# Performance work log

Hardware: AMD Instinct MI355X
Metric: run time of the kernel (lower is better)

The kernel has to match this reference:

```python
import jax, jax.numpy as jnp
import numpy as np

B, S, D, H = 2, 2048, 1024, 16
HD = D // H


def setup_inputs() -> dict:
    key = jax.random.key(0)
    ks = jax.random.split(key, 9)
    std = 0.02
    return {
        "x": jax.random.normal(ks[0], (B, S, D), dtype=jnp.float32),
        "wq": jax.random.normal(ks[1], (D, D), dtype=jnp.float32) * std,
        "bq": jnp.zeros((D,), dtype=jnp.float32),
        "wk": jax.random.normal(ks[2], (D, D), dtype=jnp.float32) * std,
        "bk": jnp.zeros((D,), dtype=jnp.float32),
        "wv": jax.random.normal(ks[3], (D, D), dtype=jnp.float32) * std,
        "bv": jnp.zeros((D,), dtype=jnp.float32),
        "wo": jax.random.normal(ks[4], (D, D), dtype=jnp.float32) * std,
        "bo": jnp.zeros((D,), dtype=jnp.float32),
    }


def reference(x, wq, bq, wk, bk, wv, bv, wo, bo):
    bsz, seq_len, d_model = x.shape
    # projections: torch Linear computes x @ W.T + b with W of shape (out, in)
    q = (x @ wq.T + bq).reshape(bsz, seq_len, H, HD).transpose(0, 2, 1, 3)  # bhsd
    k = (x @ wk.T + bk).reshape(bsz, seq_len, H, HD).transpose(0, 2, 1, 3)
    v = (x @ wv.T + bv).reshape(bsz, seq_len, H, HD).transpose(0, 2, 1, 3)
    scale = HD ** -0.5
    scores = jnp.einsum("bhqd,bhkd->bhqk", q, k) * scale  # [B,H,S,S]
    causal = jnp.tril(jnp.ones((seq_len, seq_len), dtype=bool))
    scores = jnp.where(causal[None, None], scores, -jnp.inf)
    attn = jax.nn.softmax(scores, axis=-1)
    ctx = jnp.einsum("bhqk,bhkd->bhqd", attn, v)
    ctx = ctx.transpose(0, 2, 1, 3).reshape(bsz, seq_len, d_model)
    return ctx @ wo.T + bo
```

## Files before the change

### kernel.cpp

```cpp
#include <hip/hip_runtime.h>
#include <hip/hip_bf16.h>

#define B_  2
#define S_  2048
#define D_  1024
#define H_  16
#define HD_ 64
#define M_  (B_ * S_)

typedef __bf16 bf16;
typedef __bf16 bf16x8 __attribute__((ext_vector_type(8)));
typedef float  f32x4  __attribute__((ext_vector_type(4)));

__device__ __forceinline__ bf16x8 ld8g(const bf16* p) { return *(const bf16x8*)p; }

#define GLL(g, l) __builtin_amdgcn_global_load_lds( \
    (const __attribute__((address_space(1))) void*)(g), \
    (__attribute__((address_space(3))) void*)(l), 16, 0, 0)

__global__ __launch_bounds__(256) void convert_kernel(
    const float* __restrict__ x,  const float* __restrict__ wq,
    const float* __restrict__ wk, const float* __restrict__ wv,
    const float* __restrict__ wo,
    bf16* __restrict__ xb,  bf16* __restrict__ wqb, bf16* __restrict__ wkb,
    bf16* __restrict__ wvb, bf16* __restrict__ wob)
{
    const int seg = blockIdx.y;
    const float* src;
    bf16* dst;
    if (seg < 4)      { src = x  + (long)seg * 1048576; dst = xb  + (long)seg * 1048576; }
    else if (seg == 4){ src = wq; dst = wqb; }
    else if (seg == 5){ src = wk; dst = wkb; }
    else if (seg == 6){ src = wv; dst = wvb; }
    else              { src = wo; dst = wob; }
    const long i = ((long)blockIdx.x * 256 + threadIdx.x) * 8;
    float4 a = *(const float4*)(src + i);
    float4 b = *(const float4*)(src + i + 4);
    bf16x8 r;
    r[0] = (bf16)a.x; r[1] = (bf16)a.y; r[2] = (bf16)a.z; r[3] = (bf16)a.w;
    r[4] = (bf16)b.x; r[5] = (bf16)b.y; r[6] = (bf16)b.z; r[7] = (bf16)b.w;
    *(bf16x8*)(dst + i) = r;
}

template <typename TOUT>
__device__ __forceinline__ void gemm_core(
    const bf16* __restrict__ A, const bf16* __restrict__ Bt,
    const float* __restrict__ bias, TOUT* __restrict__ Cout)
{
    __shared__ bf16 As[128 * 32];
    __shared__ bf16 Bs[128 * 32];

    const int tid  = threadIdx.x;
    const int wave = tid >> 6;
    const int lane = tid & 63;
    const int quad = lane >> 4;
    const int l15  = lane & 15;
    const int wr   = (wave >> 1) * 64;
    const int wc   = (wave & 1) * 64;
    const int m0   = blockIdx.y * 128;
    const int n0   = blockIdx.x * 128;

    const int sr = wave * 16 + (lane >> 2);
    const int sc = (lane & 3) * 8;
    const bf16* Ag = A  + (long)(m0 + sr) * D_ + sc;
    const bf16* Bg = Bt + (long)(n0 + sr) * D_ + sc;
    bf16* lA = As + wave * 512;
    bf16* lB = Bs + wave * 512;

    f32x4 acc[4][4] = {};

    for (int k0 = 0; k0 < D_; k0 += 32) {
        __syncthreads();
        GLL(Ag + k0,             lA);
        GLL(Ag + 64 * D_ + k0,   lA + 64 * 32);
        GLL(Bg + k0,             lB);
        GLL(Bg + 64 * D_ + k0,   lB + 64 * 32);
        __syncthreads();

        bf16x8 af[4], bfr[4];
        for (int mi = 0; mi < 4; mi++)
            af[mi] = *(const bf16x8*)&As[(wr + mi * 16 + l15) * 32 + quad * 8];
        for (int ni = 0; ni < 4; ni++)
            bfr[ni] = *(const bf16x8*)&Bs[(wc + ni * 16 + l15) * 32 + quad * 8];

        for (int mi = 0; mi < 4; mi++)
            for (int ni = 0; ni < 4; ni++)
                acc[mi][ni] = __builtin_amdgcn_mfma_f32_16x16x32_bf16(
                    af[mi], bfr[ni], acc[mi][ni], 0, 0, 0);
    }

    for (int ni = 0; ni < 4; ni++) {
        const int col = n0 + wc + ni * 16 + l15;
        const float bv = bias[col];
        for (int mi = 0; mi < 4; mi++) {
            const int rowb = m0 + wr + mi * 16 + quad * 4;
            for (int r = 0; r < 4; r++)
                Cout[(long)(rowb + r) * D_ + col] = (TOUT)(acc[mi][ni][r] + bv);
        }
    }
}

__global__ __launch_bounds__(256) void gemm_qkv(
    const bf16* __restrict__ xb,
    const bf16* __restrict__ wqb, const bf16* __restrict__ wkb, const bf16* __restrict__ wvb,
    const float* __restrict__ bq, const float* __restrict__ bk, const float* __restrict__ bv,
    bf16* __restrict__ qb, bf16* __restrict__ kb, bf16* __restrict__ vb)
{
    const bf16*  W  = (blockIdx.z == 0) ? wqb : (blockIdx.z == 1) ? wkb : wvb;
    const float* bi = (blockIdx.z == 0) ? bq  : (blockIdx.z == 1) ? bk  : bv;
    bf16*        o  = (blockIdx.z == 0) ? qb  : (blockIdx.z == 1) ? kb  : vb;
    gemm_core<bf16>(xb, W, bi, o);
}

__global__ __launch_bounds__(256) void gemm_out(
    const bf16* __restrict__ cb, const bf16* __restrict__ wob,
    const float* __restrict__ bo, float* __restrict__ out)
{
    gemm_core<float>(cb, wob, bo, out);
}

__global__ __launch_bounds__(256) void transpose_v(
    const bf16* __restrict__ vb, bf16* __restrict__ vt)
{
    __shared__ bf16 T[64 * 72];
    const int tid = threadIdx.x;
    const int bh  = blockIdx.y;
    const int st  = blockIdx.x;
    const int b   = bh >> 4, h = bh & 15;

    const bf16* src = vb + ((long)b * S_ + st * 64) * D_ + h * 64;
    const int r = tid >> 3;
    const int c = (tid & 7) * 8;
    bf16x8 u0 = ld8g(src + (long)r * D_ + c);
    bf16x8 u1 = ld8g(src + (long)(r + 32) * D_ + c);
    *(bf16x8*)&T[r * 72 + c]        = u0;
    *(bf16x8*)&T[(r + 32) * 72 + c] = u1;
    __syncthreads();

    for (int pass = 0; pass < 2; pass++) {
        const int hd = (tid >> 3) + pass * 32;
        const int s0 = (tid & 7) * 8;
        bf16x8 o;
        for (int e = 0; e < 8; e++) o[e] = T[(s0 + e) * 72 + hd];
        *(bf16x8*)&vt[((long)bh * 64 + hd) * S_ + st * 64 + s0] = o;
    }
}

__global__ __launch_bounds__(512) void attn_kernel(
    const bf16* __restrict__ Q, const bf16* __restrict__ K,
    const bf16* __restrict__ vt, bf16* __restrict__ ctx)
{
    constexpr int LDK = 72;
    __shared__ bf16 Ks[64 * LDK];
    __shared__ bf16 Vt[64 * LDK];
    __shared__ bf16 Pq[8][16 * LDK];

    const int tid  = threadIdx.x;
    const int wave = tid >> 6;
    const int lane = tid & 63;
    const int quad = lane >> 4;
    const int l15  = lane & 15;
    const int bh   = blockIdx.y;
    const int b    = bh >> 4, h = bh & 15;
    const long base  = ((long)b * S_) * D_ + h * HD_;
    const bf16* Vth  = vt + (long)bh * 64 * S_;

    const int krow = tid >> 3;
    const int kcol = (tid & 7) * 8;

    for (int phase = 0; phase < 2; phase++) {
        const int qt = phase ? (15 - blockIdx.x) : blockIdx.x;
        const int qw    = qt * 128 + wave * 16;
        const int qrow  = qw + l15;
        const bf16* Qr = Q + base + (long)qrow * D_;
        bf16x8 qf0 = ld8g(&Qr[quad * 8]);
        bf16x8 qf1 = ld8g(&Qr[quad * 8 + 32]);

        float l_i = 0.f;
        f32x4 o_acc[4] = {};

        bf16x8 k0 = ld8g(K + base + (long)krow * D_ + kcol);
        bf16x8 w0 = ld8g(Vth + (long)krow * S_ + kcol);

        const int njt = 2 * qt + 2;
        for (int j = 0; j < njt; j++) {
            const int kbase = j * 64;
            __syncthreads();
            *(bf16x8*)&Ks[krow * LDK + kcol] = k0;
            *(bf16x8*)&Vt[krow * LDK + kcol] = w0;
            __syncthreads();

            if (j + 1 < njt) {
                k0 = ld8g(K + base + (long)(kbase + 64 + krow) * D_ + kcol);
                w0 = ld8g(Vth + (long)krow * S_ + kbase + 64 + kcol);
            }

            if (kbase <= qw + 15) {
                f32x4 sc[4];
                for (int kt = 0; kt < 4; kt++) {
                    const bf16* Kr = &Ks[(kt * 16 + l15) * LDK + quad * 8];
                    bf16x8 a0 = *(const bf16x8*)Kr;
                    bf16x8 a1 = *(const bf16x8*)(Kr + 32);
                    f32x4 z = {};
                    z = __builtin_amdgcn_mfma_f32_16x16x32_bf16(a0, qf0, z, 0, 0, 0);
                    z = __builtin_amdgcn_mfma_f32_16x16x32_bf16(a1, qf1, z, 0, 0, 0);
                    sc[kt] = z;
                }
                float sum = 0.f;
                if (kbase + 63 > qw) {
                    for (int kt = 0; kt < 4; kt++)
                        for (int r = 0; r < 4; r++) {
                            const int k_g = kbase + kt * 16 + quad * 4 + r;
                            const float p = (k_g <= qrow)
                                ? __expf(sc[kt][r] * 0.125f) : 0.f;
                            sc[kt][r] = p;
                            sum += p;
                        }
                } else {
                    for (int kt = 0; kt < 4; kt++)
                        for (int r = 0; r < 4; r++) {
                            const float p = __expf(sc[kt][r] * 0.125f);
                            sc[kt][r] = p;
                            sum += p;
                        }
                }
                sum += __shfl_xor(sum, 16, 64);
                sum += __shfl_xor(sum, 32, 64);
                l_i += sum;

                bf16* Pw = &Pq[wave][0];
                for (int kt = 0; kt < 4; kt++) {
                    union { uint2 u; bf16 hh[4]; } pk;
                    pk.hh[0] = (bf16)sc[kt][0];
                    pk.hh[1] = (bf16)sc[kt][1];
                    pk.hh[2] = (bf16)sc[kt][2];
                    pk.hh[3] = (bf16)sc[kt][3];
                    *(uint2*)&Pw[l15 * LDK + kt * 16 + quad * 4] = pk.u;
                }
                __asm__ volatile("s_waitcnt lgkmcnt(0)" ::: "memory");
                bf16x8 pf0 = *(const bf16x8*)&Pw[l15 * LDK + quad * 8];
                bf16x8 pf1 = *(const bf16x8*)&Pw[l15 * LDK + quad * 8 + 32];

                for (int ni = 0; ni < 4; ni++) {
                    const bf16* Vr = &Vt[(ni * 16 + l15) * LDK + quad * 8];
                    bf16x8 av0 = *(const bf16x8*)Vr;
                    bf16x8 av1 = *(const bf16x8*)(Vr + 32);
                    o_acc[ni] = __builtin_amdgcn_mfma_f32_16x16x32_bf16(av0, pf0, o_acc[ni], 0, 0, 0);
                    o_acc[ni] = __builtin_amdgcn_mfma_f32_16x16x32_bf16(av1, pf1, o_acc[ni], 0, 0, 0);
                }
            }
        }

        const float invl = 1.f / l_i;
        bf16* Pw = &Pq[wave][0];
        for (int ni = 0; ni < 4; ni++)
            for (int r = 0; r < 4; r++)
                Pw[l15 * LDK + ni * 16 + quad * 4 + r] = (bf16)(o_acc[ni][r] * invl);
        __asm__ volatile("s_waitcnt lgkmcnt(0)" ::: "memory");
        for (int round = 0; round < 2; round++) {
            const int rowq = (lane >> 3) + round * 8;
            bf16x8 val = *(const bf16x8*)&Pw[rowq * LDK + (lane & 7) * 8];
            const int q_g = qt * 128 + wave * 16 + rowq;
            *(bf16x8*)&ctx[base + (long)q_g * D_ + (lane & 7) * 8] = val;
        }
    }
}

extern "C" void kernel_launch(void* const* d_in, const int* in_sizes, int n_in,
                              void* d_out, int out_size, void* d_ws, size_t ws_size,
                              hipStream_t stream)
{
    const float* x  = (const float*)d_in[0];
    const float* wq = (const float*)d_in[1];
    const float* bq = (const float*)d_in[2];
    const float* wk = (const float*)d_in[3];
    const float* bk = (const float*)d_in[4];
    const float* wv = (const float*)d_in[5];
    const float* bv = (const float*)d_in[6];
    const float* wo = (const float*)d_in[7];
    const float* bo = (const float*)d_in[8];
    float* out = (float*)d_out;

    const long NX = (long)M_ * D_;
    const long NW = (long)D_ * D_;
    bf16* xb  = (bf16*)d_ws;
    bf16* wqb = xb  + NX;
    bf16* wkb = wqb + NW;
    bf16* wvb = wkb + NW;
    bf16* wob = wvb + NW;
    bf16* qb  = wob + NW;
    bf16* kb  = qb  + NX;
    bf16* vb  = kb  + NX;
    bf16* vt  = vb  + NX;
    bf16* cb  = xb;

    dim3 blk(256, 1, 1);

    convert_kernel<<<dim3(512, 8), blk, 0, stream>>>(
        x, wq, wk, wv, wo, xb, wqb, wkb, wvb, wob);

    gemm_qkv<<<dim3(8, 32, 3), blk, 0, stream>>>(
        xb, wqb, wkb, wvb, bq, bk, bv, qb, kb, vb);

    transpose_v<<<dim3(32, 32), blk, 0, stream>>>(vb, vt);

    attn_kernel<<<dim3(8, 32), dim3(512, 1, 1), 0, stream>>>(qb, kb, vt, cb);

    gemm_out<<<dim3(8, 32), blk, 0, stream>>>(cb, wob, bo, out);
}
```

Baseline: 192.1 us.

## Fuse V transpose into QKV GEMM epilogue and split attention q-tiles across blocks

The QKV GEMM epilogue for the V projection now writes its output directly in the head-major transposed layout that attention consumes. This removes the separate transpose kernel and its extra round trip through a V buffer. The attention grid also doubles to 16 blocks along x, each handling a single q-tile instead of a balanced pair of q-tiles. Tile order is reversed for the second half of batch-heads to spread causal work. The trade-offs are strided 8-byte stores in the V epilogue and per-block work imbalance in exchange for more resident blocks.

```diff
diff --git a/kernel.cpp b/kernel.cpp
--- a/kernel.cpp
+++ b/kernel.cpp
@@ -9,6 +9,7 @@
 #define M_  (B_ * S_)
 
 typedef __bf16 bf16;
+typedef __bf16 bf16x4 __attribute__((ext_vector_type(4)));
 typedef __bf16 bf16x8 __attribute__((ext_vector_type(8)));
 typedef float  f32x4  __attribute__((ext_vector_type(4)));
 
@@ -42,13 +43,17 @@
     *(bf16x8*)(dst + i) = r;
 }
 
-template <typename TOUT>
-__device__ __forceinline__ void gemm_core(
-    const bf16* __restrict__ A, const bf16* __restrict__ Bt,
-    const float* __restrict__ bias, TOUT* __restrict__ Cout)
+__global__ __launch_bounds__(256) void gemm_qkv(
+    const bf16* __restrict__ xb,
+    const bf16* __restrict__ wqb, const bf16* __restrict__ wkb, const bf16* __restrict__ wvb,
+    const float* __restrict__ bq, const float* __restrict__ bk, const float* __restrict__ bv,
+    bf16* __restrict__ qb, bf16* __restrict__ kb, bf16* __restrict__ vt)
 {
     __shared__ bf16 As[128 * 32];
     __shared__ bf16 Bs[128 * 32];
+
+    const bf16*  Bt   = (blockIdx.z == 0) ? wqb : (blockIdx.z == 1) ? wkb : wvb;
+    const float* bias = (blockIdx.z == 0) ? bq  : (blockIdx.z == 1) ? bk  : bv;
 
     const int tid  = threadIdx.x;
     const int wave = tid >> 6;
@@ -62,7 +67,7 @@
 
     const int sr = wave * 16 + (lane >> 2);
     const int sc = (lane & 3) * 8;
-    const bf16* Ag = A  + (long)(m0 + sr) * D_ + sc;
+    const bf16* Ag = xb + (long)(m0 + sr) * D_ + sc;
     const bf16* Bg = Bt + (long)(n0 + sr) * D_ + sc;
     bf16* lA = As + wave * 512;
     bf16* lB = Bs + wave * 512;
@@ -89,60 +94,88 @@
                     af[mi], bfr[ni], acc[mi][ni], 0, 0, 0);
     }
 
+    if (blockIdx.z < 2) {
+        bf16* Cout = (blockIdx.z == 0) ? qb : kb;
+        for (int ni = 0; ni < 4; ni++) {
+            const int col = n0 + wc + ni * 16 + l15;
+            const float bv = bias[col];
+            for (int mi = 0; mi < 4; mi++) {
+                const int rowb = m0 + wr + mi * 16 + quad * 4;
+                for (int r = 0; r < 4; r++)
+                    Cout[(long)(rowb + r) * D_ + col] = (bf16)(acc[mi][ni][r] + bv);
+            }
+        }
+    } else {
+        for (int ni = 0; ni < 4; ni++) {
+            const int col = n0 + wc + ni * 16 + l15;
+            const float bv = bias[col];
+            const int h = col >> 6, hd = col & (HD_ - 1);
+            for (int mi = 0; mi < 4; mi++) {
+                const int rowb = m0 + wr + mi * 16 + quad * 4;
+                const int b = rowb >> 11;
+                const int s0 = rowb & (S_ - 1);
+                bf16x4 v4;
+                for (int r = 0; r < 4; r++) v4[r] = (bf16)(acc[mi][ni][r] + bv);
+                *(bf16x4*)&vt[(((long)(b * H_ + h)) * HD_ + hd) * S_ + s0] = v4;
+            }
+        }
+    }
+}
+
+__global__ __launch_bounds__(256) void gemm_out(
+    const bf16* __restrict__ cb, const bf16* __restrict__ wob,
+    const float* __restrict__ bo, float* __restrict__ out)
+{
+    __shared__ bf16 As[128 * 32];
+    __shared__ bf16 Bs[128 * 32];
+
+    const int tid  = threadIdx.x;
+    const int wave = tid >> 6;
+    const int lane = tid & 63;
+    const int quad = lane >> 4;
+    const int l15  = lane & 15;
+    const int wr   = (wave >> 1) * 64;
+    const int wc   = (wave & 1) * 64;
+    const int m0   = blockIdx.y * 128;
+    const int n0   = blockIdx.x * 128;
+
+    const int sr = wave * 16 + (lane >> 2);
+    const int sc = (lane & 3) * 8;
+    const bf16* Ag = cb  + (long)(m0 + sr) * D_ + sc;
+    const bf16* Bg = wob + (long)(n0 + sr) * D_ + sc;
+    bf16* lA = As + wave * 512;
+    bf16* lB = Bs + wave * 512;
+
+    f32x4 acc[4][4] = {};
+
+    for (int k0 = 0; k0 < D_; k0 += 32) {
+        __syncthreads();
+        GLL(Ag + k0,             lA);
+        GLL(Ag + 64 * D_ + k0,   lA + 64 * 32);
+        GLL(Bg + k0,             lB);
+        GLL(Bg + 64 * D_ + k0,   lB + 64 * 32);
+        __syncthreads();
+
+        bf16x8 af[4], bfr[4];
+        for (int mi = 0; mi < 4; mi++)
+            af[mi] = *(const bf16x8*)&As[(wr + mi * 16 + l15) * 32 + quad * 8];
+        for (int ni = 0; ni < 4; ni++)
+            bfr[ni] = *(const bf16x8*)&Bs[(wc + ni * 16 + l15) * 32 + quad * 8];
+
+        for (int mi = 0; mi < 4; mi++)
+            for (int ni = 0; ni < 4; ni++)
+                acc[mi][ni] = __builtin_amdgcn_mfma_f32_16x16x32_bf16(
+                    af[mi], bfr[ni], acc[mi][ni], 0, 0, 0);
+    }
+
     for (int ni = 0; ni < 4; ni++) {
         const int col = n0 + wc + ni * 16 + l15;
-        const float bv = bias[col];
+        const float bv = bo[col];
         for (int mi = 0; mi < 4; mi++) {
             const int rowb = m0 + wr + mi * 16 + quad * 4;
             for (int r = 0; r < 4; r++)
-                Cout[(long)(rowb + r) * D_ + col] = (TOUT)(acc[mi][ni][r] + bv);
-        }
-    }
-}
-
-__global__ __launch_bounds__(256) void gemm_qkv(
-    const bf16* __restrict__ xb,
-    const bf16* __restrict__ wqb, const bf16* __restrict__ wkb, const bf16* __restrict__ wvb,
-    const float* __restrict__ bq, const float* __restrict__ bk, const float* __restrict__ bv,
-    bf16* __restrict__ qb, bf16* __restrict__ kb, bf16* __restrict__ vb)
-{
-    const bf16*  W  = (blockIdx.z == 0) ? wqb : (blockIdx.z == 1) ? wkb : wvb;
-    const float* bi = (blockIdx.z == 0) ? bq  : (blockIdx.z == 1) ? bk  : bv;
-    bf16*        o  = (blockIdx.z == 0) ? qb  : (blockIdx.z == 1) ? kb  : vb;
-    gemm_core<bf16>(xb, W, bi, o);
-}
-
-__global__ __launch_bounds__(256) void gemm_out(
-    const bf16* __restrict__ cb, const bf16* __restrict__ wob,
-    const float* __restrict__ bo, float* __restrict__ out)
-{
-    gemm_core<float>(cb, wob, bo, out);
-}
-
-__global__ __launch_bounds__(256) void transpose_v(
-    const bf16* __restrict__ vb, bf16* __restrict__ vt)
-{
-    __shared__ bf16 T[64 * 72];
-    const int tid = threadIdx.x;
-    const int bh  = blockIdx.y;
-    const int st  = blockIdx.x;
-    const int b   = bh >> 4, h = bh & 15;
-
-    const bf16* src = vb + ((long)b * S_ + st * 64) * D_ + h * 64;
-    const int r = tid >> 3;
-    const int c = (tid & 7) * 8;
-    bf16x8 u0 = ld8g(src + (long)r * D_ + c);
-    bf16x8 u1 = ld8g(src + (long)(r + 32) * D_ + c);
-    *(bf16x8*)&T[r * 72 + c]        = u0;
-    *(bf16x8*)&T[(r + 32) * 72 + c] = u1;
-    __syncthreads();
-
-    for (int pass = 0; pass < 2; pass++) {
-        const int hd = (tid >> 3) + pass * 32;
-        const int s0 = (tid & 7) * 8;
-        bf16x8 o;
-        for (int e = 0; e < 8; e++) o[e] = T[(s0 + e) * 72 + hd];
-        *(bf16x8*)&vt[((long)bh * 64 + hd) * S_ + st * 64 + s0] = o;
+                out[(long)(rowb + r) * D_ + col] = acc[mi][ni][r] + bv;
+        }
     }
 }
 
@@ -161,108 +194,106 @@
     const int quad = lane >> 4;
     const int l15  = lane & 15;
     const int bh   = blockIdx.y;
+    const int qt   = (blockIdx.y < 16) ? blockIdx.x : (15 - (int)blockIdx.x);
     const int b    = bh >> 4, h = bh & 15;
     const long base  = ((long)b * S_) * D_ + h * HD_;
-    const bf16* Vth  = vt + (long)bh * 64 * S_;
+    const bf16* Vth  = vt + (long)bh * HD_ * S_;
 
     const int krow = tid >> 3;
     const int kcol = (tid & 7) * 8;
 
-    for (int phase = 0; phase < 2; phase++) {
-        const int qt = phase ? (15 - blockIdx.x) : blockIdx.x;
-        const int qw    = qt * 128 + wave * 16;
-        const int qrow  = qw + l15;
-        const bf16* Qr = Q + base + (long)qrow * D_;
-        bf16x8 qf0 = ld8g(&Qr[quad * 8]);
-        bf16x8 qf1 = ld8g(&Qr[quad * 8 + 32]);
-
-        float l_i = 0.f;
-        f32x4 o_acc[4] = {};
-
-        bf16x8 k0 = ld8g(K + base + (long)krow * D_ + kcol);
-        bf16x8 w0 = ld8g(Vth + (long)krow * S_ + kcol);
-
-        const int njt = 2 * qt + 2;
-        for (int j = 0; j < njt; j++) {
-            const int kbase = j * 64;
-            __syncthreads();
-            *(bf16x8*)&Ks[krow * LDK + kcol] = k0;
-            *(bf16x8*)&Vt[krow * LDK + kcol] = w0;
-            __syncthreads();
-
-            if (j + 1 < njt) {
-                k0 = ld8g(K + base + (long)(kbase + 64 + krow) * D_ + kcol);
-                w0 = ld8g(Vth + (long)krow * S_ + kbase + 64 + kcol);
-            }
-
-            if (kbase <= qw + 15) {
-                f32x4 sc[4];
-                for (int kt = 0; kt < 4; kt++) {
-                    const bf16* Kr = &Ks[(kt * 16 + l15) * LDK + quad * 8];
-                    bf16x8 a0 = *(const bf16x8*)Kr;
-                    bf16x8 a1 = *(const bf16x8*)(Kr + 32);
-                    f32x4 z = {};
-                    z = __builtin_amdgcn_mfma_f32_16x16x32_bf16(a0, qf0, z, 0, 0, 0);
-                    z = __builtin_amdgcn_mfma_f32_16x16x32_bf16(a1, qf1, z, 0, 0, 0);
-                    sc[kt] = z;
-                }
-                float sum = 0.f;
-                if (kbase + 63 > qw) {
-                    for (int kt = 0; kt < 4; kt++)
-                        for (int r = 0; r < 4; r++) {
-                            const int k_g = kbase + kt * 16 + quad * 4 + r;
-                            const float p = (k_g <= qrow)
-                                ? __expf(sc[kt][r] * 0.125f) : 0.f;
-                            sc[kt][r] = p;
-                            sum += p;
-                        }
-                } else {
-                    for (int kt = 0; kt < 4; kt++)
-                        for (int r = 0; r < 4; r++) {
-                            const float p = __expf(sc[kt][r] * 0.125f);
-                            sc[kt][r] = p;
-                            sum += p;
-                        }
-                }
-                sum += __shfl_xor(sum, 16, 64);
-                sum += __shfl_xor(sum, 32, 64);
-                l_i += sum;
-
-                bf16* Pw = &Pq[wave][0];
-                for (int kt = 0; kt < 4; kt++) {
-                    union { uint2 u; bf16 hh[4]; } pk;
-                    pk.hh[0] = (bf16)sc[kt][0];
-                    pk.hh[1] = (bf16)sc[kt][1];
-                    pk.hh[2] = (bf16)sc[kt][2];
-                    pk.hh[3] = (bf16)sc[kt][3];
-                    *(uint2*)&Pw[l15 * LDK + kt * 16 + quad * 4] = pk.u;
-                }
-                __asm__ volatile("s_waitcnt lgkmcnt(0)" ::: "memory");
-                bf16x8 pf0 = *(const bf16x8*)&Pw[l15 * LDK + quad * 8];
-                bf16x8 pf1 = *(const bf16x8*)&Pw[l15 * LDK + quad * 8 + 32];
-
-                for (int ni = 0; ni < 4; ni++) {
-                    const bf16* Vr = &Vt[(ni * 16 + l15) * LDK + quad * 8];
-                    bf16x8 av0 = *(const bf16x8*)Vr;
-                    bf16x8 av1 = *(const bf16x8*)(Vr + 32);
-                    o_acc[ni] = __builtin_amdgcn_mfma_f32_16x16x32_bf16(av0, pf0, o_acc[ni], 0, 0, 0);
-                    o_acc[ni] = __builtin_amdgcn_mfma_f32_16x16x32_bf16(av1, pf1, o_acc[ni], 0, 0, 0);
-                }
-            }
-        }
-
-        const float invl = 1.f / l_i;
-        bf16* Pw = &Pq[wave][0];
-        for (int ni = 0; ni < 4; ni++)
-            for (int r = 0; r < 4; r++)
-                Pw[l15 * LDK + ni * 16 + quad * 4 + r] = (bf16)(o_acc[ni][r] * invl);
-        __asm__ volatile("s_waitcnt lgkmcnt(0)" ::: "memory");
-        for (int round = 0; round < 2; round++) {
-            const int rowq = (lane >> 3) + round * 8;
-            bf16x8 val = *(const bf16x8*)&Pw[rowq * LDK + (lane & 7) * 8];
-            const int q_g = qt * 128 + wave * 16 + rowq;
-            *(bf16x8*)&ctx[base + (long)q_g * D_ + (lane & 7) * 8] = val;
-        }
+    const int qw    = qt * 128 + wave * 16;
+    const int qrow  = qw + l15;
+    const bf16* Qr = Q + base + (long)qrow * D_;
+    bf16x8 qf0 = ld8g(&Qr[quad * 8]);
+    bf16x8 qf1 = ld8g(&Qr[quad * 8 + 32]);
+
+    float l_i = 0.f;
+    f32x4 o_acc[4] = {};
+
+    bf16x8 k0 = ld8g(K + base + (long)krow * D_ + kcol);
+    bf16x8 w0 = ld8g(Vth + (long)krow * S_ + kcol);
+
+    const int njt = 2 * qt + 2;
+    for (int j = 0; j < njt; j++) {
+        const int kbase = j * 64;
+        __syncthreads();
+        *(bf16x8*)&Ks[krow * LDK + kcol] = k0;
+        *(bf16x8*)&Vt[krow * LDK + kcol] = w0;
+        __syncthreads();
+
+        if (j + 1 < njt) {
+            k0 = ld8g(K + base + (long)(kbase + 64 + krow) * D_ + kcol);
+            w0 = ld8g(Vth + (long)krow * S_ + kbase + 64 + kcol);
+        }
+
+        if (kbase <= qw + 15) {
+            f32x4 sc[4];
+            for (int kt = 0; kt < 4; kt++) {
+                const bf16* Kr = &Ks[(kt * 16 + l15) * LDK + quad * 8];
+                bf16x8 a0 = *(const bf16x8*)Kr;
+                bf16x8 a1 = *(const bf16x8*)(Kr + 32);
+                f32x4 z = {};
+                z = __builtin_amdgcn_mfma_f32_16x16x32_bf16(a0, qf0, z, 0, 0, 0);
+                z = __builtin_amdgcn_mfma_f32_16x16x32_bf16(a1, qf1, z, 0, 0, 0);
+                sc[kt] = z;
+            }
+            float sum = 0.f;
+            if (kbase + 63 > qw) {
+                for (int kt = 0; kt < 4; kt++)
+                    for (int r = 0; r < 4; r++) {
+                        const int k_g = kbase + kt * 16 + quad * 4 + r;
+                        const float p = (k_g <= qrow)
+                            ? __expf(sc[kt][r] * 0.125f) : 0.f;
+                        sc[kt][r] = p;
+                        sum += p;
+                    }
+            } else {
+                for (int kt = 0; kt < 4; kt++)
+                    for (int r = 0; r < 4; r++) {
+                        const float p = __expf(sc[kt][r] * 0.125f);
+                        sc[kt][r] = p;
+                        sum += p;
+                    }
+            }
+            sum += __shfl_xor(sum, 16, 64);
+            sum += __shfl_xor(sum, 32, 64);
+            l_i += sum;
+
+            bf16* Pw = &Pq[wave][0];
+            for (int kt = 0; kt < 4; kt++) {
+                union { uint2 u; bf16 hh[4]; } pk;
+                pk.hh[0] = (bf16)sc[kt][0];
+                pk.hh[1] = (bf16)sc[kt][1];
+                pk.hh[2] = (bf16)sc[kt][2];
+                pk.hh[3] = (bf16)sc[kt][3];
+                *(uint2*)&Pw[l15 * LDK + kt * 16 + quad * 4] = pk.u;
+            }
+            __asm__ volatile("s_waitcnt lgkmcnt(0)" ::: "memory");
+            bf16x8 pf0 = *(const bf16x8*)&Pw[l15 * LDK + quad * 8];
+            bf16x8 pf1 = *(const bf16x8*)&Pw[l15 * LDK + quad * 8 + 32];
+
+            for (int ni = 0; ni < 4; ni++) {
+                const bf16* Vr = &Vt[(ni * 16 + l15) * LDK + quad * 8];
+                bf16x8 av0 = *(const bf16x8*)Vr;
+                bf16x8 av1 = *(const bf16x8*)(Vr + 32);
+                o_acc[ni] = __builtin_amdgcn_mfma_f32_16x16x32_bf16(av0, pf0, o_acc[ni], 0, 0, 0);
+                o_acc[ni] = __builtin_amdgcn_mfma_f32_16x16x32_bf16(av1, pf1, o_acc[ni], 0, 0, 0);
+            }
+        }
+    }
+
+    const float invl = 1.f / l_i;
+    bf16* Pw = &Pq[wave][0];
+    for (int ni = 0; ni < 4; ni++)
+        for (int r = 0; r < 4; r++)
+            Pw[l15 * LDK + ni * 16 + quad * 4 + r] = (bf16)(o_acc[ni][r] * invl);
+    __asm__ volatile("s_waitcnt lgkmcnt(0)" ::: "memory");
+    for (int round = 0; round < 2; round++) {
+        const int rowq = (lane >> 3) + round * 8;
+        bf16x8 val = *(const bf16x8*)&Pw[rowq * LDK + (lane & 7) * 8];
+        const int q_g = qt * 128 + wave * 16 + rowq;
+        *(bf16x8*)&ctx[base + (long)q_g * D_ + (lane & 7) * 8] = val;
     }
 }
 
@@ -290,8 +321,7 @@
     bf16* wob = wvb + NW;
     bf16* qb  = wob + NW;
     bf16* kb  = qb  + NX;
-    bf16* vb  = kb  + NX;
-    bf16* vt  = vb  + NX;
+    bf16* vt  = kb  + NX;
     bf16* cb  = xb;
 
     dim3 blk(256, 1, 1);
@@ -300,11 +330,9 @@
         x, wq, wk, wv, wo, xb, wqb, wkb, wvb, wob);
 
     gemm_qkv<<<dim3(8, 32, 3), blk, 0, stream>>>(
-        xb, wqb, wkb, wvb, bq, bk, bv, qb, kb, vb);
-
-    transpose_v<<<dim3(32, 32), blk, 0, stream>>>(vb, vt);
-
-    attn_kernel<<<dim3(8, 32), dim3(512, 1, 1), 0, stream>>>(qb, kb, vt, cb);
+        xb, wqb, wkb, wvb, bq, bk, bv, qb, kb, vt);
+
+    attn_kernel<<<dim3(16, 32), dim3(512, 1, 1), 0, stream>>>(qb, kb, vt, cb);
 
     gemm_out<<<dim3(8, 32), blk, 0, stream>>>(cb, wob, bo, out);
 }
```

Result: faster. 186.3 us (-3.1%).
